# Optimization experiments

Measured on AMD Instinct MI355X. Metric: run time of the kernel, lower is better.

Reference implementation:

```python
import jax, jax.numpy as jnp
import numpy as np

W_LEN = 8      # window_len
DEPTH = 3      # sig_depth (implementation hardcodes depth-3 truncated signature)


def _seg_exp(d):
    """Truncated tensor-exponential of a linear segment with increment d (N,D)."""
    t1 = d
    t2 = 0.5 * jnp.einsum('ni,nj->nij', d, d)
    t3 = jnp.einsum('nij,nk->nijk', t2, d) / 3.0  # d^{\otimes 3}/6
    return t1, t2, t3


def _signature_depth3(path):
    """path: (N, L, D) -> flattened depth-3 signature (N, D + D^2 + D^3),
    matching signatory.signature ordering (levels concatenated, row-major)."""
    N, L, D = path.shape
    dx = path[:, 1:] - path[:, :-1]          # (N, L-1, D) increments
    s1, s2, s3 = _seg_exp(dx[:, 0])

    def chen_step(carry, d):
        s1, s2, s3 = carry
        t1, t2, t3 = _seg_exp(d)
        n1 = s1 + t1
        n2 = s2 + jnp.einsum('ni,nj->nij', s1, t1) + t2
        n3 = (s3
              + jnp.einsum('nij,nk->nijk', s2, t1)
              + jnp.einsum('ni,njk->nijk', s1, t2)
              + t3)
        return (n1, n2, n3), None

    # scan over the remaining L-2 increments (time axis leading)
    (s1, s2, s3), _ = jax.lax.scan(chen_step, (s1, s2, s3),
                                   jnp.moveaxis(dx[:, 1:], 1, 0))
    return jnp.concatenate([s1, s2.reshape(N, -1), s3.reshape(N, -1)], axis=-1)


def _rolling_windows(x, w_len):
    """x: (B,T,D) -> (B,T,W,D); window t covers [max(0,t-W+1), t],
    left-padded by repeating the first element (clamped indices)."""
    T = x.shape[1]
    idx = jnp.clip(jnp.arange(T)[:, None] - (w_len - 1) + jnp.arange(w_len)[None, :], 0, T - 1)  # (T,W)
    return x[:, idx]  # (B,T,W,D)


def setup_inputs() -> dict:
    key = jax.random.key(0)
    k1, k2, k3 = jax.random.split(key, 3)
    B, T, D = 8, 4096, 8
    sig_channels = D + D * D + D * D * D  # 584
    proj_dim = 128
    x = jax.random.normal(k1, (B, T, D), dtype=jnp.float32)
    w_proj = jax.random.normal(k2, (sig_channels, proj_dim), dtype=jnp.float32) * (1.0 / np.sqrt(sig_channels))
    b_proj = jax.random.normal(k3, (proj_dim,), dtype=jnp.float32) * 0.01
    return {"x": x, "w_proj": w_proj, "b_proj": b_proj}


def reference(x, w_proj, b_proj):
    B, T, D = x.shape
    windows = _rolling_windows(x, W_LEN).reshape(B * T, W_LEN, D)
    sig = _signature_depth3(windows).reshape(B, T, -1)   # (B,T,584)
    return sig @ w_proj + b_proj                          # (B,T,128)
```

## Files before the change

kernel.cpp:

```cpp
#include <hip/hip_runtime.h>
#include <hip/hip_bf16.h>

typedef unsigned short ushort_t;
typedef __attribute__((ext_vector_type(8))) short short8;
typedef __attribute__((ext_vector_type(4))) float floatx4;
typedef __attribute__((ext_vector_type(4))) int intx4;

#define SIG_CH 584
#define KPAD   608
#define NPROJ  128
#define ASTRIDE 616
#define TLEN   4096
#define NWIN   32768
#define WPB    32

__device__ __forceinline__ ushort_t f2bf(float f) {
    unsigned int v; __builtin_memcpy(&v, &f, 4);
    v += 0x7fffu + ((v >> 16) & 1u);
    return (ushort_t)(v >> 16);
}

__device__ __forceinline__ ushort_t f2bf_hw(float f) {
    __hip_bfloat16 h = __float2bfloat16(f);
    ushort_t u; __builtin_memcpy(&u, &h, 2);
    return u;
}

__global__ void pack_w_kernel(const float* __restrict__ w, ushort_t* __restrict__ wp) {
    int idx = blockIdx.x * 256 + threadIdx.x;
    if (idx >= (KPAD / 8) * NPROJ) return;
    int n  = idx & (NPROJ - 1);
    int kb = idx >> 7;
    union { ushort_t u[8]; intx4 v; } pk;
    #pragma unroll
    for (int kk = 0; kk < 8; ++kk) {
        int c = kb * 8 + kk;
        pk.u[kk] = (c < SIG_CH) ? f2bf(w[c * NPROJ + n]) : (ushort_t)0;
    }
    *(intx4*)(wp + ((size_t)kb * NPROJ + n) * 8) = pk.v;
}

__launch_bounds__(256, 3)
__global__ void sig_gemm_kernel(const float* __restrict__ x,
                                const ushort_t* __restrict__ wp,
                                const float* __restrict__ bias,
                                float* __restrict__ out) {
    __shared__ __align__(16) float    s_dinc[WPB + 6][8];
    __shared__ __align__(16) ushort_t s_A[WPB][ASTRIDE];

    const int tid  = threadIdx.x;
    const int blk  = blockIdx.x;
    const int g0   = blk * WPB;
    const int b    = g0 >> 12;
    const int t0   = g0 & (TLEN - 1);

    if (tid < (WPB + 6) * 2) {
        const int h = tid & 1, r = tid >> 1;
        const int u  = t0 - 7 + r;
        const int ua = u < 0 ? 0 : u;
        const int ub = (u + 1) < 0 ? 0 : (u + 1);
        const floatx4* xb4 = (const floatx4*)(x + ((size_t)b << 15));
        ((floatx4*)s_dinc)[tid] = xb4[ub * 2 + h] - xb4[ua * 2 + h];
    }
    for (int idx = tid; idx < WPB * 32; idx += 256) {
        int r = idx >> 5, c = SIG_CH + (idx & 31);
        s_A[r][c] = 0;
    }
    __syncthreads();

    const int wv   = tid >> 6;
    const int lane = tid & 63;
    const int li   = lane >> 3;
    const int lj   = lane & 7;

    #pragma unroll 1
    for (int wp2 = 0; wp2 < 4; ++wp2) {
        const int w = wv * 8 + wp2 * 2;

        float diL[8], djL[8];
        #pragma unroll
        for (int r = 0; r < 8; ++r) {
            diL[r] = s_dinc[w + r][li];
            djL[r] = s_dinc[w + r][lj];
        }

        float hA = 0.f, gA = 0.f, s2A = 0.f;
        float hB = 0.f, gB = 0.f, s2B = 0.f;
        float s3A[8] = {0.f,0.f,0.f,0.f,0.f,0.f,0.f,0.f};
        float s3B[8] = {0.f,0.f,0.f,0.f,0.f,0.f,0.f,0.f};

        floatx4 ra0 = *(const floatx4*)(&s_dinc[w][0]);
        floatx4 ra1 = *(const floatx4*)(&s_dinc[w][4]);

        #pragma unroll
        for (int st = 0; st < 7; ++st) {
            const floatx4 rb0 = *(const floatx4*)(&s_dinc[w + st + 1][0]);
            const floatx4 rb1 = *(const floatx4*)(&s_dinc[w + st + 1][4]);
            const float diA = diL[st],     djA = djL[st];
            const float diB = diL[st + 1], djB = djL[st + 1];
            const float c3A = fmaf(djA, fmaf(0.166666667f, diA, 0.5f * hA), s2A);
            const float c3B = fmaf(djB, fmaf(0.166666667f, diB, 0.5f * hB), s2B);
            s2A = fmaf(djA, fmaf(0.5f, diA, hA), s2A);
            s2B = fmaf(djB, fmaf(0.5f, diB, hB), s2B);
            #pragma unroll
            for (int k = 0; k < 4; ++k) {
                s3A[k]     = fmaf(c3A, ra0[k], s3A[k]);
                s3A[k + 4] = fmaf(c3A, ra1[k], s3A[k + 4]);
                s3B[k]     = fmaf(c3B, rb0[k], s3B[k]);
                s3B[k + 4] = fmaf(c3B, rb1[k], s3B[k + 4]);
            }
            hA += diA; gA += djA;
            hB += diB; gB += djB;
            ra0 = rb0; ra1 = rb1;
        }

        union { ushort_t u[8]; intx4 v; } pkA, pkB;
        #pragma unroll
        for (int k = 0; k < 8; k += 2) {
            __hip_bfloat162 a2 = __float22bfloat162_rn(float2{s3A[k], s3A[k + 1]});
            __hip_bfloat162 b2 = __float22bfloat162_rn(float2{s3B[k], s3B[k + 1]});
            __builtin_memcpy(&pkA.u[k], &a2, 4);
            __builtin_memcpy(&pkB.u[k], &b2, 4);
        }
        *(intx4*)(&s_A[w][72 + lane * 8])     = pkA.v;
        *(intx4*)(&s_A[w + 1][72 + lane * 8]) = pkB.v;
        s_A[w][8 + lane]     = f2bf_hw(s2A);
        s_A[w + 1][8 + lane] = f2bf_hw(s2B);
        if (lane < 8) {
            s_A[w][lane]     = f2bf_hw(gA);
            s_A[w + 1][lane] = f2bf_hw(gB);
        }
    }
    __syncthreads();

    const int lrow  = lane & 15;
    const int kgrp  = lane >> 4;
    const int ncol0 = wv * 32 + lrow;

    floatx4 acc[2][2];
    #pragma unroll
    for (int mt = 0; mt < 2; ++mt) {
        acc[mt][0] = floatx4{0.f, 0.f, 0.f, 0.f};
        acc[mt][1] = floatx4{0.f, 0.f, 0.f, 0.f};
    }

    for (int kc = 0; kc < 19; ++kc) {
        const int kb = kc * 4 + kgrp;
        const short8 b0 = *(const short8*)(wp + ((size_t)kb * NPROJ + ncol0) * 8);
        const short8 b1 = *(const short8*)(wp + ((size_t)kb * NPROJ + ncol0 + 16) * 8);
        #pragma unroll
        for (int mt = 0; mt < 2; ++mt) {
            const short8 af = *(const short8*)(&s_A[mt * 16 + lrow][kc * 32 + kgrp * 8]);
            acc[mt][0] = __builtin_amdgcn_mfma_f32_16x16x32_bf16(af, b0, acc[mt][0], 0, 0, 0);
            acc[mt][1] = __builtin_amdgcn_mfma_f32_16x16x32_bf16(af, b1, acc[mt][1], 0, 0, 0);
        }
    }

    const float bias0 = bias[ncol0];
    const float bias1 = bias[ncol0 + 16];
    #pragma unroll
    for (int mt = 0; mt < 2; ++mt) {
        #pragma unroll
        for (int r = 0; r < 4; ++r) {
            const int row = g0 + mt * 16 + kgrp * 4 + r;
            out[(size_t)row * NPROJ + ncol0]      = acc[mt][0][r] + bias0;
            out[(size_t)row * NPROJ + ncol0 + 16] = acc[mt][1][r] + bias1;
        }
    }
}

extern "C" void kernel_launch(void* const* d_in, const int* in_sizes, int n_in,
                              void* d_out, int out_size, void* d_ws, size_t ws_size,
                              hipStream_t stream) {
    const float* x  = (const float*)d_in[0];
    const float* w  = (const float*)d_in[1];
    const float* bp = (const float*)d_in[2];
    ushort_t* wp    = (ushort_t*)d_ws;
    float* out = (float*)d_out;

    const int wpk_total = (KPAD / 8) * NPROJ;
    hipLaunchKernelGGL(pack_w_kernel, dim3((wpk_total + 255) / 256), dim3(256), 0, stream,
                       w, wp);
    hipLaunchKernelGGL(sig_gemm_kernel, dim3(NWIN / WPB), dim3(256), 0, stream,
                       x, wp, bp, out);
}
```

Before: 75.80 us.

## Fuse weight bf16 packing into the signature GEMM kernel and drop the pack launch

Removes the separate kernel that packed the fp32 projection weights into bf16. The main kernel now reads fp32 weights straight from global memory, converts them to bf16 in registers, and prefetches the next K-chunk in software while the current chunk's MFMAs run. This saves one kernel launch and the workspace round-trip. In exchange, every block reloads the weights at twice the byte size through many scalar strided loads and repeats the conversion, which adds L2 traffic and VALU work inside the GEMM loop.

```diff
diff --git a/kernel.cpp b/kernel.cpp
--- a/kernel.cpp
+++ b/kernel.cpp
@@ -7,18 +7,11 @@
 typedef __attribute__((ext_vector_type(4))) int intx4;
 
 #define SIG_CH 584
-#define KPAD   608
 #define NPROJ  128
 #define ASTRIDE 616
 #define TLEN   4096
 #define NWIN   32768
 #define WPB    32
-
-__device__ __forceinline__ ushort_t f2bf(float f) {
-    unsigned int v; __builtin_memcpy(&v, &f, 4);
-    v += 0x7fffu + ((v >> 16) & 1u);
-    return (ushort_t)(v >> 16);
-}
 
 __device__ __forceinline__ ushort_t f2bf_hw(float f) {
     __hip_bfloat16 h = __float2bfloat16(f);
@@ -26,25 +19,11 @@
     return u;
 }
 
-__global__ void pack_w_kernel(const float* __restrict__ w, ushort_t* __restrict__ wp) {
-    int idx = blockIdx.x * 256 + threadIdx.x;
-    if (idx >= (KPAD / 8) * NPROJ) return;
-    int n  = idx & (NPROJ - 1);
-    int kb = idx >> 7;
-    union { ushort_t u[8]; intx4 v; } pk;
-    #pragma unroll
-    for (int kk = 0; kk < 8; ++kk) {
-        int c = kb * 8 + kk;
-        pk.u[kk] = (c < SIG_CH) ? f2bf(w[c * NPROJ + n]) : (ushort_t)0;
-    }
-    *(intx4*)(wp + ((size_t)kb * NPROJ + n) * 8) = pk.v;
-}
-
 __launch_bounds__(256, 3)
-__global__ void sig_gemm_kernel(const float* __restrict__ x,
-                                const ushort_t* __restrict__ wp,
-                                const float* __restrict__ bias,
-                                float* __restrict__ out) {
+__global__ void sig_gemm_fused(const float* __restrict__ x,
+                               const float* __restrict__ w,
+                               const float* __restrict__ bias,
+                               float* __restrict__ out) {
     __shared__ __align__(16) float    s_dinc[WPB + 6][8];
     __shared__ __align__(16) ushort_t s_A[WPB][ASTRIDE];
 
@@ -75,13 +54,13 @@
 
     #pragma unroll 1
     for (int wp2 = 0; wp2 < 4; ++wp2) {
-        const int w = wv * 8 + wp2 * 2;
+        const int w_ = wv * 8 + wp2 * 2;
 
         float diL[8], djL[8];
         #pragma unroll
         for (int r = 0; r < 8; ++r) {
-            diL[r] = s_dinc[w + r][li];
-            djL[r] = s_dinc[w + r][lj];
+            diL[r] = s_dinc[w_ + r][li];
+            djL[r] = s_dinc[w_ + r][lj];
         }
 
         float hA = 0.f, gA = 0.f, s2A = 0.f;
@@ -89,13 +68,13 @@
         float s3A[8] = {0.f,0.f,0.f,0.f,0.f,0.f,0.f,0.f};
         float s3B[8] = {0.f,0.f,0.f,0.f,0.f,0.f,0.f,0.f};
 
-        floatx4 ra0 = *(const floatx4*)(&s_dinc[w][0]);
-        floatx4 ra1 = *(const floatx4*)(&s_dinc[w][4]);
+        floatx4 ra0 = *(const floatx4*)(&s_dinc[w_][0]);
+        floatx4 ra1 = *(const floatx4*)(&s_dinc[w_][4]);
 
         #pragma unroll
         for (int st = 0; st < 7; ++st) {
-            const floatx4 rb0 = *(const floatx4*)(&s_dinc[w + st + 1][0]);
-            const floatx4 rb1 = *(const floatx4*)(&s_dinc[w + st + 1][4]);
+            const floatx4 rb0 = *(const floatx4*)(&s_dinc[w_ + st + 1][0]);
+            const floatx4 rb1 = *(const floatx4*)(&s_dinc[w_ + st + 1][4]);
             const float diA = diL[st],     djA = djL[st];
             const float diB = diL[st + 1], djB = djL[st + 1];
             const float c3A = fmaf(djA, fmaf(0.166666667f, diA, 0.5f * hA), s2A);
@@ -122,13 +101,13 @@
             __builtin_memcpy(&pkA.u[k], &a2, 4);
             __builtin_memcpy(&pkB.u[k], &b2, 4);
         }
-        *(intx4*)(&s_A[w][72 + lane * 8])     = pkA.v;
-        *(intx4*)(&s_A[w + 1][72 + lane * 8]) = pkB.v;
-        s_A[w][8 + lane]     = f2bf_hw(s2A);
-        s_A[w + 1][8 + lane] = f2bf_hw(s2B);
+        *(intx4*)(&s_A[w_][72 + lane * 8])     = pkA.v;
+        *(intx4*)(&s_A[w_ + 1][72 + lane * 8]) = pkB.v;
+        s_A[w_][8 + lane]     = f2bf_hw(s2A);
+        s_A[w_ + 1][8 + lane] = f2bf_hw(s2B);
         if (lane < 8) {
-            s_A[w][lane]     = f2bf_hw(gA);
-            s_A[w + 1][lane] = f2bf_hw(gB);
+            s_A[w_][lane]     = f2bf_hw(gA);
+            s_A[w_ + 1][lane] = f2bf_hw(gB);
         }
     }
     __syncthreads();
@@ -136,6 +115,8 @@
     const int lrow  = lane & 15;
     const int kgrp  = lane >> 4;
     const int ncol0 = wv * 32 + lrow;
+    const float* w0 = w + ncol0;
+    const float* w1 = w + ncol0 + 16;
 
     floatx4 acc[2][2];
     #pragma unroll
@@ -144,15 +125,40 @@
         acc[mt][1] = floatx4{0.f, 0.f, 0.f, 0.f};
     }
 
+    float pf0[8], pf1[8];
+    {
+        const int k0 = kgrp * 8;
+        #pragma unroll
+        for (int kk = 0; kk < 8; ++kk) {
+            pf0[kk] = w0[(size_t)(k0 + kk) * NPROJ];
+            pf1[kk] = w1[(size_t)(k0 + kk) * NPROJ];
+        }
+    }
+
+    #pragma unroll 1
     for (int kc = 0; kc < 19; ++kc) {
-        const int kb = kc * 4 + kgrp;
-        const short8 b0 = *(const short8*)(wp + ((size_t)kb * NPROJ + ncol0) * 8);
-        const short8 b1 = *(const short8*)(wp + ((size_t)kb * NPROJ + ncol0 + 16) * 8);
+        union { ushort_t u[8]; short8 s8; } c0, c1;
+        #pragma unroll
+        for (int kk = 0; kk < 8; kk += 2) {
+            __hip_bfloat162 p0 = __float22bfloat162_rn(float2{pf0[kk], pf0[kk + 1]});
+            __hip_bfloat162 p1 = __float22bfloat162_rn(float2{pf1[kk], pf1[kk + 1]});
+            __builtin_memcpy(&c0.u[kk], &p0, 4);
+            __builtin_memcpy(&c1.u[kk], &p1, 4);
+        }
+        if (kc < 18) {
+            const int kn = (kc + 1) * 32 + kgrp * 8;
+            const bool ok = (kn + 7) < SIG_CH;
+            #pragma unroll
+            for (int kk = 0; kk < 8; ++kk) {
+                pf0[kk] = ok ? w0[(size_t)(kn + kk) * NPROJ] : 0.f;
+                pf1[kk] = ok ? w1[(size_t)(kn + kk) * NPROJ] : 0.f;
+            }
+        }
         #pragma unroll
         for (int mt = 0; mt < 2; ++mt) {
             const short8 af = *(const short8*)(&s_A[mt * 16 + lrow][kc * 32 + kgrp * 8]);
-            acc[mt][0] = __builtin_amdgcn_mfma_f32_16x16x32_bf16(af, b0, acc[mt][0], 0, 0, 0);
-            acc[mt][1] = __builtin_amdgcn_mfma_f32_16x16x32_bf16(af, b1, acc[mt][1], 0, 0, 0);
+            acc[mt][0] = __builtin_amdgcn_mfma_f32_16x16x32_bf16(af, c0.s8, acc[mt][0], 0, 0, 0);
+            acc[mt][1] = __builtin_amdgcn_mfma_f32_16x16x32_bf16(af, c1.s8, acc[mt][1], 0, 0, 0);
         }
     }
 
@@ -175,12 +181,9 @@
     const float* x  = (const float*)d_in[0];
     const float* w  = (const float*)d_in[1];
     const float* bp = (const float*)d_in[2];
-    ushort_t* wp    = (ushort_t*)d_ws;
     float* out = (float*)d_out;
+    (void)d_ws; (void)ws_size;
 
-    const int wpk_total = (KPAD / 8) * NPROJ;
-    hipLaunchKernelGGL(pack_w_kernel, dim3((wpk_total + 255) / 256), dim3(256), 0, stream,
-                       w, wp);
-    hipLaunchKernelGGL(sig_gemm_kernel, dim3(NWIN / WPB), dim3(256), 0, stream,
-                       x, wp, bp, out);
+    hipLaunchKernelGGL(sig_gemm_fused, dim3(NWIN / WPB), dim3(256), 0, stream,
+                       x, w, bp, out);
 }
```

New measurement: 81.13 us. 7.0% more time.
